# Optimization experiments

Hardware: AMD Instinct MI355X
Metric: run time of the kernel (lower is better)

## Reference

```python
import jax, jax.numpy as jnp
import numpy as np
import math

B, S, E, H = 2, 2048, 768, 12
D = E // H            # head_dim = 64
FFN = 3072            # GeGLU hidden
WIN = 64              # local window size
GLOBAL_IDS = np.array([0])
EPS = 1e-5


def _rope(x):
    # x: [B,H,S,D]; interleaved rotary embedding, theta=10000 (lucidrains RotaryEmbedding)
    d = x.shape[-1]
    s = x.shape[-2]
    inv_freq = 1.0 / (10000.0 ** (jnp.arange(0, d, 2, dtype=jnp.float32) / d))
    freqs = jnp.arange(s, dtype=jnp.float32)[:, None] * inv_freq[None, :]  # [S, D/2]
    freqs = jnp.repeat(freqs, 2, axis=-1)                                   # [S, D]
    cos, sin = jnp.cos(freqs), jnp.sin(freqs)
    xp = x.reshape(x.shape[:-1] + (d // 2, 2))
    x_rot = jnp.stack([-xp[..., 1], xp[..., 0]], axis=-1).reshape(x.shape)
    return x * cos + x_rot * sin


def _layernorm(x, scale, bias):
    mu = jnp.mean(x, axis=-1, keepdims=True)
    var = jnp.mean(jnp.square(x - mu), axis=-1, keepdims=True)
    return (x - mu) * jax.lax.rsqrt(var + EPS) * scale + bias


def setup_inputs() -> dict:
    key = jax.random.key(0)
    ks = jax.random.split(key, 10)
    def xav(k, shape, gain):
        fan_out, fan_in = shape
        std = gain * math.sqrt(2.0 / (fan_in + fan_out))
        return jax.random.normal(k, shape, jnp.float32) * std
    g2 = math.sqrt(2.0)
    g13 = math.sqrt(1.0 / 3.0)
    return {
        "x": jax.random.normal(ks[0], (B, S, E), jnp.float32),
        "rel_pos_bias": jax.random.normal(ks[1], (B, S, S), jnp.float32),
        "mask": jnp.ones((B, S), dtype=bool),
        "wq_w": xav(ks[2], (E, E), g2), "wq_b": jnp.zeros((E,), jnp.float32),
        "wk_w": xav(ks[3], (E, E), g2), "wk_b": jnp.zeros((E,), jnp.float32),
        "wv_w": xav(ks[4], (E, E), g2), "wv_b": jnp.zeros((E,), jnp.float32),
        "fc_w": xav(ks[5], (E, E), g2), "fc_b": jnp.zeros((E,), jnp.float32),
        "pos_coeff": jnp.full((H, 1, 1), 0.01, jnp.float32),
        "gate_w": xav(ks[6], (FFN, E), g13), "gate_b": jnp.zeros((FFN,), jnp.float32),
        "value_w": xav(ks[7], (FFN, E), g2), "value_b": jnp.zeros((FFN,), jnp.float32),
        "down_w": xav(ks[8], (E, FFN), g2), "down_b": jnp.zeros((E,), jnp.float32),
        "ln1_s": jnp.ones((E,), jnp.float32), "ln1_b": jnp.zeros((E,), jnp.float32),
        "ln2_s": jnp.ones((E,), jnp.float32), "ln2_b": jnp.zeros((E,), jnp.float32),
    }


def _sparse_allow(mask):
    # static local-window + global-token pattern, [S,S] bool
    idx = jnp.arange(S)
    allow = jnp.abs(idx[:, None] - idx[None, :]) <= WIN
    gidx = jnp.asarray(GLOBAL_IDS)
    allow = allow.at[gidx, :].set(True)
    allow = allow.at[:, gidx].set(True)
    # combine with padding mask [B,S] broadcast over query rows
    return allow[None, None, :, :] & mask[:, None, None, :]  # [B,1,S,S]


def reference(x, rel_pos_bias, mask, wq_w, wq_b, wk_w, wk_b, wv_w, wv_b,
              fc_w, fc_b, pos_coeff, gate_w, gate_b, value_w, value_b,
              down_w, down_b, ln1_s, ln1_b, ln2_s, ln2_b):
    def heads(t):  # [B,S,E] -> [B,H,S,D]
        return t.reshape(B, S, H, D).transpose(0, 2, 1, 3)

    Q = _rope(heads(x @ wq_w.T + wq_b))
    K = _rope(heads(x @ wk_w.T + wk_b))
    V = heads(x @ wv_w.T + wv_b)

    scores = jnp.einsum('bhqd,bhkd->bhqk', Q, K) / math.sqrt(D)
    scores = scores + pos_coeff[None] * rel_pos_bias[:, None]     # [B,H,S,S]
    allow = _sparse_allow(mask)
    scores = jnp.where(allow, scores, -1e30)
    scores = scores - jnp.max(scores, axis=-1, keepdims=True)
    attn = jax.nn.softmax(scores, axis=-1)
    ctx = jnp.einsum('bhqk,bhkd->bhqd', attn, V)
    ctx = ctx.transpose(0, 2, 1, 3).reshape(B, S, E)
    attn_out = ctx @ fc_w.T + fc_b

    h = _layernorm(x + attn_out, ln1_s, ln1_b)
    gate = jax.nn.gelu(h @ gate_w.T + gate_b, approximate=False)
    ffn = (gate * (h @ value_w.T + value_b)) @ down_w.T + down_b
    return _layernorm(h + ffn, ln2_s, ln2_b)
```

## Files before the change

### kernel.cpp

```cpp
#include <hip/hip_runtime.h>
#include <math.h>

#define B_   2
#define S_   2048
#define E_   768
#define H_   12
#define D_   64
#define FFN_ 3072
#define WIN_ 64
#define MTOT (B_*S_)

typedef unsigned short ushort_t;
typedef unsigned short ushort8 __attribute__((ext_vector_type(8)));
typedef __bf16 bf16x8 __attribute__((ext_vector_type(8)));
typedef float f32x4 __attribute__((ext_vector_type(4)));

__device__ __forceinline__ float b2f(ushort_t u) {
    union { unsigned int i; float f; } c; c.i = ((unsigned int)u) << 16; return c.f;
}
__device__ __forceinline__ ushort_t f2b(float f) {
    union { float f; unsigned int i; } c; c.f = f;
    unsigned int u = c.i;
    return (ushort_t)((u + 0x7fffu + ((u >> 16) & 1u)) >> 16);
}
__device__ __forceinline__ float gelu_f(float g) {
    return 0.5f * g * (1.f + erff(g * 0.70710678118654752440f));
}

typedef const __attribute__((address_space(1))) void* gptr_t;
typedef __attribute__((address_space(3))) void* lptr_t;
__device__ __forceinline__ void gload16(const void* g, void* l) {
    __builtin_amdgcn_global_load_lds((gptr_t)g,
        (lptr_t)(unsigned int)(unsigned long long)l, 16, 0, 0);
}

__global__ __launch_bounds__(256)
void cvt_f32_bf16(const float* __restrict__ in, ushort_t* __restrict__ out, int n8)
{
    const int idx = blockIdx.x * 256 + threadIdx.x;
    if (idx >= n8) return;
    const float4* p = (const float4*)(in + (size_t)idx * 8);
    const float4 a = p[0], b = p[1];
    ushort8 o;
    o[0]=f2b(a.x); o[1]=f2b(a.y); o[2]=f2b(a.z); o[3]=f2b(a.w);
    o[4]=f2b(b.x); o[5]=f2b(b.y); o[6]=f2b(b.z); o[7]=f2b(b.w);
    *(ushort8*)(out + (size_t)idx*8) = o;
}

__global__ __launch_bounds__(256)
void cvt_interleave(const float* __restrict__ gw, const float* __restrict__ vw,
                    ushort_t* __restrict__ out)
{
    const int idx = blockIdx.x*256 + threadIdx.x;
    const int R   = idx / 96, c8 = idx - R*96;
    const int blk = R >> 6, w = R & 63;
    const float* src = (w < 32 ? gw : vw) + (size_t)(blk*32 + (w & 31))*768 + c8*8;
    const float4 a = ((const float4*)src)[0], b = ((const float4*)src)[1];
    ushort8 o;
    o[0]=f2b(a.x); o[1]=f2b(a.y); o[2]=f2b(a.z); o[3]=f2b(a.w);
    o[4]=f2b(b.x); o[5]=f2b(b.y); o[6]=f2b(b.z); o[7]=f2b(b.w);
    *(ushort8*)(out + (size_t)idx*8) = o;
}

__global__ __launch_bounds__(256)
void rope_table(float2* __restrict__ ctab)
{
    const int idx = blockIdx.x*256 + threadIdx.x;
    if (idx >= S_*32) return;
    const int s = idx >> 5, i = idx & 31;
    const float inv = exp2f(-(float)i * (13.287712379549449f/32.0f));
    const float fr = (float)s * inv;
    ctab[idx] = make_float2(cosf(fr), sinf(fr));
}

__global__ __launch_bounds__(256)
void rope_apply(ushort_t* __restrict__ Qb, ushort_t* __restrict__ Kb,
                const float2* __restrict__ ctab)
{
    const int NP4 = MTOT*E_/8;
    int idx = blockIdx.x*256 + threadIdx.x;
    ushort_t* ptr = Qb;
    if (idx >= NP4) { ptr = Kb; idx -= NP4; if (idx >= NP4) return; }
    const size_t p0 = (size_t)idx * 4;
    const int e2 = (int)(p0 % (E_/2));
    const int s  = (int)((p0 / (E_/2)) % S_);
    const int i0 = e2 & 31;
    ushort8 v = *(ushort8*)(ptr + p0*2);
    ushort8 o;
#pragma unroll
    for (int t = 0; t < 4; ++t) {
        const float2 cs = ctab[s*32 + i0 + t];
        const float x0 = b2f(v[2*t]), x1 = b2f(v[2*t+1]);
        o[2*t]   = f2b(x0*cs.x - x1*cs.y);
        o[2*t+1] = f2b(x1*cs.x + x0*cs.y);
    }
    *(ushort8*)(ptr + p0*2) = o;
}

template<int EPI, int BN>
__global__ __launch_bounds__(256)
void gemm_mfma(const ushort_t* __restrict__ A,
               const ushort_t* W0, const float* b0, void* C0,
               const ushort_t* W1, const float* b1, void* C1,
               const ushort_t* W2, const float* b2, void* C2,
               const void* __restrict__ aux, int M, int N, int K)
{
    constexpr int NWC = BN/64, NWR = 4/NWC, WROWS = 128/NWR, MF = WROWS/16;
    const ushort_t* W = W0; const float* bias = b0; void* C = C0;
    if (blockIdx.z == 1) { W = W1; bias = b1; C = C1; }
    else if (blockIdx.z == 2) { W = W2; bias = b2; C = C2; }

    __shared__ __align__(16) ushort_t As[128*32];
    __shared__ __align__(16) ushort_t Bs[BN*32];

    const int tid = threadIdx.x, wv = tid>>6, lane = tid&63;
    const int m0 = blockIdx.y*128, n0 = blockIdx.x*BN;
    const int wr = wv / NWC, wc = wv % NWC;
    const int lr16 = lane & 15, lkb = (lane>>4)<<3;

    f32x4 acc[MF][4];
#pragma unroll
    for (int i=0;i<MF;++i)
#pragma unroll
        for (int j=0;j<4;++j) acc[i][j] = f32x4{0.f,0.f,0.f,0.f};

    const char* Ab = (const char*)(A + (size_t)m0*K);
    const char* Wb = (const char*)(W + (size_t)n0*K);
    const size_t rb = (size_t)K*2;
    const int wbase = wv*1024, lby = lane*16;

    for (int kt = 0; kt < K; kt += 32) {
        const size_t kb = (size_t)kt*2;
        int n_ = wbase + lby;
        gload16(Ab + (size_t)(n_>>6)*rb + kb + (n_&63), (char*)As + wbase);
        n_ += 4096;
        gload16(Ab + (size_t)(n_>>6)*rb + kb + (n_&63), (char*)As + wbase + 4096);
        n_ = wbase + lby;
        gload16(Wb + (size_t)(n_>>6)*rb + kb + (n_&63), (char*)Bs + wbase);
        if (BN == 128) {
            n_ += 4096;
            gload16(Wb + (size_t)(n_>>6)*rb + kb + (n_&63), (char*)Bs + wbase + 4096);
        }
        __syncthreads();
        bf16x8 af[MF], bfr[4];
#pragma unroll
        for (int mf=0; mf<MF; ++mf)
            af[mf] = *(const bf16x8*)&As[(wr*WROWS + mf*16 + lr16)*32 + lkb];
#pragma unroll
        for (int nf=0; nf<4; ++nf)
            bfr[nf] = *(const bf16x8*)&Bs[(wc*64 + nf*16 + lr16)*32 + lkb];
#pragma unroll
        for (int mf=0; mf<MF; ++mf)
#pragma unroll
            for (int nf=0; nf<4; ++nf)
                acc[mf][nf] = __builtin_amdgcn_mfma_f32_16x16x32_bf16(af[mf], bfr[nf], acc[mf][nf], 0,0,0);
        __syncthreads();
    }

    const int colb = n0 + wc*64 + lr16;
    const int rowb = m0 + wr*WROWS + ((lane>>4)<<2);
#pragma unroll
    for (int nf=0; nf<4; ++nf) {
        const int col = colb + nf*16;
        const float bsv = bias[col];
#pragma unroll
        for (int mf=0; mf<MF; ++mf) {
            const int row = rowb + mf*16;
            const f32x4 a = acc[mf][nf];
#pragma unroll
            for (int r=0; r<4; ++r) {
                const size_t off = (size_t)(row+r)*N + col;
                const float v = a[r] + bsv;
                if constexpr (EPI == 0) {
                    ((ushort_t*)C)[off] = f2b(v);
                } else if constexpr (EPI == 1) {
                    ((float*)C)[off] = v + ((const float*)aux)[off];
                } else {
                    if (blockIdx.z == 2) {
                        const int rr = row + r;
                        const size_t toff =
                            (((size_t)(rr >> 11)*H_ + (col >> 6))*64 + (col & 63))*(size_t)S_ + (rr & (S_-1));
                        ((ushort_t*)C)[toff] = f2b(v);
                    } else {
                        ((ushort_t*)C)[off] = f2b(v);
                    }
                }
            }
        }
    }
}

__global__ __launch_bounds__(256, 2)
void gemm_geglu(const ushort_t* __restrict__ A,
                const ushort_t* __restrict__ Wgv,
                const float* __restrict__ bgp,
                const float* __restrict__ bvp,
                ushort_t* __restrict__ C)
{
    constexpr int NT   = 12;
    constexpr int ABY  = 128*128;
    constexpr int BUFB = 2*ABY;
    __shared__ __align__(16) char lds[2*BUFB];

    const int id  = blockIdx.x;
    const int stI = (id & 7)*3 + ((id >> 3) >> 6);
    const int w64 = (id >> 3) & 63;
    const int gy  = (stI/6)*8 + (w64 >> 3);
    const int gx  = (stI%6)*8 + (w64 & 7);
    const int m0 = gy*128, n0 = gx*128;

    const int tid = threadIdx.x, wv = tid>>6, l = tid&63;
    const int wr = wv>>1, wc = wv&1;
    const int lr16 = l & 15, g16b = (l>>4)<<4;
    const int xr = (lr16 & 7) << 4;

    const int lrow = l >> 3;
    const int swzc = ((l & 7) ^ lrow) << 4;
    const char* Agp = (const char*)A   + (size_t)(m0 + wv*32 + lrow)*1536 + swzc;
    const char* Bgp = (const char*)Wgv + (size_t)(n0 + wv*32 + lrow)*1536 + swzc;

    const int rA0 = (wr*64 +  0 + lr16)*128, rA1 = (wr*64 + 16 + lr16)*128;
    const int rA2 = (wr*64 + 32 + lr16)*128, rA3 = (wr*64 + 48 + lr16)*128;
    const int rB0 = ABY + (wc*64 +  0 + lr16)*128, rB1 = ABY + (wc*64 + 16 + lr16)*128;
    const int rB2 = ABY + (wc*64 + 32 + lr16)*128, rB3 = ABY + (wc*64 + 48 + lr16)*128;
    const int ck0 = g16b ^ xr, ck1 = (64 + g16b) ^ xr;

    f32x4 acc[4][4];
#pragma unroll
    for (int i=0;i<4;++i)
#pragma unroll
        for (int j=0;j<4;++j) acc[i][j] = f32x4{0.f,0.f,0.f,0.f};

#define STG(tt, cb) { \
    char* dA = lds + (cb)*BUFB + wv*4096; \
    char* dB = lds + (cb)*BUFB + ABY + wv*4096; \
    const size_t ko = (size_t)(tt)*128; \
    gload16(Agp + ko,           dA); \
    gload16(Agp + ko +  8*1536, dA + 1024); \
    gload16(Agp + ko + 16*1536, dA + 2048); \
    gload16(Agp + ko + 24*1536, dA + 3072); \
    gload16(Bgp + ko,           dB); \
    gload16(Bgp + ko +  8*1536, dB + 1024); \
    gload16(Bgp + ko + 16*1536, dB + 2048); \
    gload16(Bgp + ko + 24*1536, dB + 3072); }

    STG(0, 0);
    __syncthreads();

    int c = 0;
#pragma unroll 1
    for (int t = 0; t < NT; ++t) {
        if (t < NT-1) STG(t+1, c^1);
        const char* Lb = lds + c*BUFB;
        const bf16x8 a0 = *(const bf16x8*)(Lb + rA0 + ck0);
        const bf16x8 a1 = *(const bf16x8*)(Lb + rA1 + ck0);
        const bf16x8 a2 = *(const bf16x8*)(Lb + rA2 + ck0);
        const bf16x8 a3 = *(const bf16x8*)(Lb + rA3 + ck0);
        const bf16x8 b0 = *(const bf16x8*)(Lb + rB0 + ck0);
        const bf16x8 b1 = *(const bf16x8*)(Lb + rB1 + ck0);
        const bf16x8 b2 = *(const bf16x8*)(Lb + rB2 + ck0);
        const bf16x8 b3 = *(const bf16x8*)(Lb + rB3 + ck0);
        const bf16x8 e0 = *(const bf16x8*)(Lb + rA0 + ck1);
        const bf16x8 e1 = *(const bf16x8*)(Lb + rA1 + ck1);
        const bf16x8 e2 = *(const bf16x8*)(Lb + rA2 + ck1);
        const bf16x8 e3 = *(const bf16x8*)(Lb + rA3 + ck1);
        const bf16x8 f0 = *(const bf16x8*)(Lb + rB0 + ck1);
        const bf16x8 f1 = *(const bf16x8*)(Lb + rB1 + ck1);
        const bf16x8 f2 = *(const bf16x8*)(Lb + rB2 + ck1);
        const bf16x8 f3 = *(const bf16x8*)(Lb + rB3 + ck1);
        __builtin_amdgcn_s_setprio(1);
        acc[0][0] = __builtin_amdgcn_mfma_f32_16x16x32_bf16(a0, b0, acc[0][0], 0,0,0);
        acc[1][0] = __builtin_amdgcn_mfma_f32_16x16x32_bf16(a1, b0, acc[1][0], 0,0,0);
        acc[2][0] = __builtin_amdgcn_mfma_f32_16x16x32_bf16(a2, b0, acc[2][0], 0,0,0);
        acc[3][0] = __builtin_amdgcn_mfma_f32_16x16x32_bf16(a3, b0, acc[3][0], 0,0,0);
        acc[0][1] = __builtin_amdgcn_mfma_f32_16x16x32_bf16(a0, b1, acc[0][1], 0,0,0);
        acc[1][1] = __builtin_amdgcn_mfma_f32_16x16x32_bf16(a1, b1, acc[1][1], 0,0,0);
        acc[2][1] = __builtin_amdgcn_mfma_f32_16x16x32_bf16(a2, b1, acc[2][1], 0,0,0);
        acc[3][1] = __builtin_amdgcn_mfma_f32_16x16x32_bf16(a3, b1, acc[3][1], 0,0,0);
        acc[0][2] = __builtin_amdgcn_mfma_f32_16x16x32_bf16(a0, b2, acc[0][2], 0,0,0);
        acc[1][2] = __builtin_amdgcn_mfma_f32_16x16x32_bf16(a1, b2, acc[1][2], 0,0,0);
        acc[2][2] = __builtin_amdgcn_mfma_f32_16x16x32_bf16(a2, b2, acc[2][2], 0,0,0);
        acc[3][2] = __builtin_amdgcn_mfma_f32_16x16x32_bf16(a3, b2, acc[3][2], 0,0,0);
        acc[0][3] = __builtin_amdgcn_mfma_f32_16x16x32_bf16(a0, b3, acc[0][3], 0,0,0);
        acc[1][3] = __builtin_amdgcn_mfma_f32_16x16x32_bf16(a1, b3, acc[1][3], 0,0,0);
        acc[2][3] = __builtin_amdgcn_mfma_f32_16x16x32_bf16(a2, b3, acc[2][3], 0,0,0);
        acc[3][3] = __builtin_amdgcn_mfma_f32_16x16x32_bf16(a3, b3, acc[3][3], 0,0,0);
        acc[0][0] = __builtin_amdgcn_mfma_f32_16x16x32_bf16(e0, f0, acc[0][0], 0,0,0);
        acc[1][0] = __builtin_amdgcn_mfma_f32_16x16x32_bf16(e1, f0, acc[1][0], 0,0,0);
        acc[2][0] = __builtin_amdgcn_mfma_f32_16x16x32_bf16(e2, f0, acc[2][0], 0,0,0);
        acc[3][0] = __builtin_amdgcn_mfma_f32_16x16x32_bf16(e3, f0, acc[3][0], 0,0,0);
        acc[0][1] = __builtin_amdgcn_mfma_f32_16x16x32_bf16(e0, f1, acc[0][1], 0,0,0);
        acc[1][1] = __builtin_amdgcn_mfma_f32_16x16x32_bf16(e1, f1, acc[1][1], 0,0,0);
        acc[2][1] = __builtin_amdgcn_mfma_f32_16x16x32_bf16(e2, f1, acc[2][1], 0,0,0);
        acc[3][1] = __builtin_amdgcn_mfma_f32_16x16x32_bf16(e3, f1, acc[3][1], 0,0,0);
        acc[0][2] = __builtin_amdgcn_mfma_f32_16x16x32_bf16(e0, f2, acc[0][2], 0,0,0);
        acc[1][2] = __builtin_amdgcn_mfma_f32_16x16x32_bf16(e1, f2, acc[1][2], 0,0,0);
        acc[2][2] = __builtin_amdgcn_mfma_f32_16x16x32_bf16(e2, f2, acc[2][2], 0,0,0);
        acc[3][2] = __builtin_amdgcn_mfma_f32_16x16x32_bf16(e3, f2, acc[3][2], 0,0,0);
        acc[0][3] = __builtin_amdgcn_mfma_f32_16x16x32_bf16(e0, f3, acc[0][3], 0,0,0);
        acc[1][3] = __builtin_amdgcn_mfma_f32_16x16x32_bf16(e1, f3, acc[1][3], 0,0,0);
        acc[2][3] = __builtin_amdgcn_mfma_f32_16x16x32_bf16(e2, f3, acc[2][3], 0,0,0);
        acc[3][3] = __builtin_amdgcn_mfma_f32_16x16x32_bf16(e3, f3, acc[3][3], 0,0,0);
        __builtin_amdgcn_s_setprio(0);
        __syncthreads();
        c ^= 1;
    }
#undef STG

    const int colb = gx*64 + wc*32 + lr16;
    const int rowb = m0 + wr*64 + ((l>>4)<<2);
#pragma unroll
    for (int nf=0; nf<2; ++nf) {
        const int col = colb + nf*16;
        const float bgv = bgp[col], bvv = bvp[col];
#pragma unroll
        for (int mf=0; mf<4; ++mf) {
            const int row = rowb + mf*16;
            const f32x4 gq = acc[mf][nf];
            const f32x4 vq = acc[mf][nf+2];
#pragma unroll
            for (int r=0; r<4; ++r) {
                C[(size_t)(row+r)*3072 + col] =
                    f2b(gelu_f(gq[r] + bgv) * (vq[r] + bvv));
            }
        }
    }
}

__global__ __launch_bounds__(256)
void attn_mfma(const ushort_t* __restrict__ Qb, const ushort_t* __restrict__ Kb,
               const ushort_t* __restrict__ Vt, const float* __restrict__ rel,
               const float* __restrict__ pos_coeff, ushort_t* __restrict__ ctx)
{
    __shared__ __align__(16) ushort_t P_lds[4][16][160];
    const int id = blockIdx.x;
    const int h  = id % H_;
    const int qb = (id / H_) & 31;
    const int b  = id / (H_*32);
    const int wv = threadIdx.x >> 6, l = threadIdx.x & 63;
    const int qw = qb*64 + wv*16;
    const int g  = l >> 4, ql = l & 15;
    const int q  = qw + ql;

    int klo = qw - 64;
    if (klo < 0) klo = 0;
    if (klo > S_-160) klo = S_-160;
    const bool addg = (klo > 0);
    const float pc = pos_coeff[h];

    const ushort_t* qbp = Qb + ((size_t)(b*S_ + qw))*E_ + h*D_ + (size_t)ql*E_ + g*8;
    const bf16x8 qf0 = *(const bf16x8*)(qbp);
    const bf16x8 qf1 = *(const bf16x8*)(qbp + 32);

    float sg = -1e30f, pg = 0.f;
    const float* relrow = rel + ((size_t)(b*S_ + q))*S_;
    if (addg) {
        const ushort_t* k0p = Kb + (size_t)(b*S_)*E_ + h*D_ + g*8;
        const bf16x8 k00 = *(const bf16x8*)(k0p);
        const bf16x8 k01 = *(const bf16x8*)(k0p + 32);
        float part = 0.f;
#pragma unroll
        for (int t = 0; t < 8; ++t) {
            part = fmaf((float)k00[t], (float)qf0[t], part);
            part = fmaf((float)k01[t], (float)qf1[t], part);
        }
        part += __shfl_xor(part, 16);
        part += __shfl_xor(part, 32);
        sg = part*0.125f + pc*relrow[0];
    }

    f32x4 sc_[10];
#pragma unroll
    for (int f = 0; f < 10; ++f) sc_[f] = f32x4{0.f,0.f,0.f,0.f};
    const ushort_t* kbp = Kb + ((size_t)(b*S_ + klo))*E_ + h*D_;
#pragma unroll
    for (int f = 0; f < 10; ++f) {
        const ushort_t* kr = kbp + (size_t)(16*f + ql)*E_ + g*8;
        const bf16x8 kf0 = *(const bf16x8*)(kr);
        const bf16x8 kf1 = *(const bf16x8*)(kr + 32);
        sc_[f] = __builtin_amdgcn_mfma_f32_16x16x32_bf16(kf0, qf0, sc_[f], 0,0,0);
        sc_[f] = __builtin_amdgcn_mfma_f32_16x16x32_bf16(kf1, qf1, sc_[f], 0,0,0);
    }

#pragma unroll
    for (int f = 0; f < 10; ++f) {
#pragma unroll
        for (int r = 0; r < 4; ++r) {
            const int slot = 16*f + 4*g + r;
            const int key  = klo + slot;
            const int dd   = key - q;
            const bool ok  = (dd <= WIN_ && dd >= -WIN_) || (key == 0);
            const float v  = sc_[f][r]*0.125f + pc*relrow[key];
            sc_[f][r] = ok ? v : -1e30f;
        }
    }

    float mx = sg;
#pragma unroll
    for (int f = 0; f < 10; ++f)
#pragma unroll
        for (int r = 0; r < 4; ++r) mx = fmaxf(mx, sc_[f][r]);
    mx = fmaxf(mx, __shfl_xor(mx, 16));
    mx = fmaxf(mx, __shfl_xor(mx, 32));

    float ls = 0.f;
#pragma unroll
    for (int f = 0; f < 10; ++f)
#pragma unroll
        for (int r = 0; r < 4; ++r) {
            const float p = __expf(sc_[f][r] - mx);
            sc_[f][r] = p; ls += p;
        }
    if (addg) pg = __expf(sg - mx);
    ls += (g == 0) ? pg : 0.f;
    ls += __shfl_xor(ls, 16);
    ls += __shfl_xor(ls, 32);
    const float inv = 1.f / ls;

#pragma unroll
    for (int f = 0; f < 10; ++f)
#pragma unroll
        for (int r = 0; r < 4; ++r)
            P_lds[wv][ql][16*f + 4*g + r] = f2b(sc_[f][r]);
    __syncthreads();

    f32x4 acc_c[4];
#pragma unroll
    for (int df = 0; df < 4; ++df) acc_c[df] = f32x4{0.f,0.f,0.f,0.f};
    const ushort_t* vtb = Vt + ((size_t)(b*H_ + h)*64)*(size_t)S_;
#pragma unroll
    for (int s5 = 0; s5 < 5; ++s5) {
        const bf16x8 pf = *(const bf16x8*)&P_lds[wv][ql][32*s5 + 8*g];
#pragma unroll
        for (int df = 0; df < 4; ++df) {
            const bf16x8 vtf = *(const bf16x8*)(vtb + (size_t)(df*16 + ql)*S_ + klo + 32*s5 + g*8);
            acc_c[df] = __builtin_amdgcn_mfma_f32_16x16x32_bf16(vtf, pf, acc_c[df], 0,0,0);
        }
    }

    if (addg) {
#pragma unroll
        for (int df = 0; df < 4; ++df)
#pragma unroll
            for (int r = 0; r < 4; ++r)
                acc_c[df][r] = fmaf(pg, b2f(vtb[(size_t)(df*16 + g*4 + r)*S_]), acc_c[df][r]);
    }

    if (q != 0) {
        ushort_t* cb = ctx + ((size_t)(b*S_ + q))*E_ + h*D_;
#pragma unroll
        for (int df = 0; df < 4; ++df)
#pragma unroll
            for (int r = 0; r < 4; ++r)
                cb[df*16 + g*4 + r] = f2b(acc_c[df][r] * inv);
    }
}

__global__ __launch_bounds__(256)
void attn_global(const ushort_t* __restrict__ Qb, const ushort_t* __restrict__ Kb,
                 const ushort_t* __restrict__ Vt, const float* __restrict__ rel,
                 const float* __restrict__ pos_coeff, ushort_t* __restrict__ ctx)
{
    __shared__ float sc[S_];
    __shared__ float sq[D_];
    __shared__ float red[4];
    __shared__ float pacc[4][D_];
    const int tid = threadIdx.x, wv = tid>>6, lane = tid&63;
    const int id = blockIdx.x, h = id % H_, b = id / H_;

    if (tid < 64) sq[tid] = b2f(Qb[(size_t)(b*S_)*E_ + h*D_ + tid]);
    __syncthreads();

    const float pc = pos_coeff[h];
    const ushort_t* kbase = Kb + (size_t)b*S_*E_ + h*D_;
    const float* relrow = rel + (size_t)b*S_*S_;
    const int g = lane >> 2, sl = lane & 3;

    for (int jb = wv*16; jb < S_; jb += 64) {
        const int j = jb + g;
        const ushort_t* kr = kbase + (size_t)j*E_ + sl*16;
        const ushort8 k0 = *(const ushort8*)kr;
        const ushort8 k1 = *(const ushort8*)(kr + 8);
        const float* qv = &sq[sl*16];
        float partial = 0.f;
#pragma unroll
        for (int t = 0; t < 8; ++t) partial = fmaf(b2f(k0[t]), qv[t], partial);
#pragma unroll
        for (int t = 0; t < 8; ++t) partial = fmaf(b2f(k1[t]), qv[t+8], partial);
        partial += __shfl_xor(partial, 1);
        partial += __shfl_xor(partial, 2);
        if (sl == 0) sc[j] = partial*0.125f + pc*relrow[j];
    }
    __syncthreads();

    float mx = -1e30f;
#pragma unroll
    for (int i = 0; i < 8; ++i) mx = fmaxf(mx, sc[tid + 256*i]);
#pragma unroll
    for (int off = 32; off > 0; off >>= 1) mx = fmaxf(mx, __shfl_xor(mx, off));
    if (lane == 0) red[wv] = mx;
    __syncthreads();
    mx = fmaxf(fmaxf(red[0], red[1]), fmaxf(red[2], red[3]));

    float sum = 0.f;
#pragma unroll
    for (int i = 0; i < 8; ++i) {
        const float p = __expf(sc[tid + 256*i] - mx);
        sc[tid + 256*i] = p; sum += p;
    }
#pragma unroll
    for (int off = 32; off > 0; off >>= 1) sum += __shfl_xor(sum, off);
    __syncthreads();
    if (lane == 0) red[wv] = sum;
    __syncthreads();
    const float inv = 1.f / (red[0]+red[1]+red[2]+red[3]);

    const ushort_t* vtrow = Vt + ((size_t)(b*H_ + h)*64 + lane)*(size_t)S_;
    float acc = 0.f;
    for (int j0 = wv*512; j0 < wv*512 + 512; j0 += 8) {
        const ushort8 v8 = *(const ushort8*)&vtrow[j0];
#pragma unroll
        for (int t = 0; t < 8; ++t) acc = fmaf(sc[j0+t], b2f(v8[t]), acc);
    }
    pacc[wv][lane] = acc;
    __syncthreads();
    if (tid < 64) {
        const float r = (pacc[0][tid]+pacc[1][tid]+pacc[2][tid]+pacc[3][tid]) * inv;
        ctx[(size_t)(b*S_)*E_ + h*D_ + tid] = f2b(r);
    }
}

template<bool WB>
__global__ __launch_bounds__(256)
void ln_kernel(const float* __restrict__ in, const float* __restrict__ gam,
               const float* __restrict__ bet, float* __restrict__ out,
               ushort_t* __restrict__ outb)
{
    const int row = blockIdx.x;
    const float* r = in + (size_t)row * E_;
    const int tid = threadIdx.x;
    const float v0 = r[tid], v1 = r[tid+256], v2 = r[tid+512];
    float s  = v0+v1+v2;
    float ss = v0*v0+v1*v1+v2*v2;
#pragma unroll
    for (int off = 32; off > 0; off >>= 1) {
        s  += __shfl_xor(s, off);
        ss += __shfl_xor(ss, off);
    }
    __shared__ float rs[4], rss[4];
    const int wv = tid >> 6, lane = tid & 63;
    if (lane == 0) { rs[wv] = s; rss[wv] = ss; }
    __syncthreads();
    s  = rs[0]+rs[1]+rs[2]+rs[3];
    ss = rss[0]+rss[1]+rss[2]+rss[3];
    const float mu  = s * (1.f/E_);
    const float var = ss * (1.f/E_) - mu*mu;
    const float rstd = rsqrtf(var + 1e-5f);
    float* o = out + (size_t)row * E_;
    const float o0 = (v0-mu)*rstd*gam[tid    ] + bet[tid    ];
    const float o1 = (v1-mu)*rstd*gam[tid+256] + bet[tid+256];
    const float o2 = (v2-mu)*rstd*gam[tid+512] + bet[tid+512];
    o[tid] = o0; o[tid+256] = o1; o[tid+512] = o2;
    if constexpr (WB) {
        ushort_t* ob = outb + (size_t)row * E_;
        ob[tid] = f2b(o0); ob[tid+256] = f2b(o1); ob[tid+512] = f2b(o2);
    }
}

extern "C" void kernel_launch(void* const* d_in, const int* in_sizes, int n_in,
                              void* d_out, int out_size, void* d_ws, size_t ws_size,
                              hipStream_t stream)
{
    const float* x      = (const float*)d_in[0];
    const float* rel    = (const float*)d_in[1];
    const float* wq_w   = (const float*)d_in[3];
    const float* wq_b   = (const float*)d_in[4];
    const float* wk_w   = (const float*)d_in[5];
    const float* wk_b   = (const float*)d_in[6];
    const float* wv_w   = (const float*)d_in[7];
    const float* wv_b   = (const float*)d_in[8];
    const float* fc_w   = (const float*)d_in[9];
    const float* fc_b   = (const float*)d_in[10];
    const float* pos_c  = (const float*)d_in[11];
    const float* gate_w = (const float*)d_in[12];
    const float* gate_b = (const float*)d_in[13];
    const float* value_w= (const float*)d_in[14];
    const float* value_b= (const float*)d_in[15];
    const float* down_w = (const float*)d_in[16];
    const float* down_b = (const float*)d_in[17];
    const float* ln1_s  = (const float*)d_in[18];
    const float* ln1_b  = (const float*)d_in[19];
    const float* ln2_s  = (const float*)d_in[20];
    const float* ln2_b  = (const float*)d_in[21];
    float* out = (float*)d_out;

    char* W = (char*)d_ws;
    ushort_t* Qb     = (ushort_t*)(W + 0);
    ushort_t* Kb     = (ushort_t*)(W + 6291456);
    ushort_t* Vt     = (ushort_t*)(W + 12582912);
    ushort_t* Cxb    = (ushort_t*)(W + 18874368);
    ushort_t* GpB    = (ushort_t*)(W + 0);
    ushort_t* Xb     = (ushort_t*)(W + 25165824);
    ushort_t* wqb    = (ushort_t*)(W + 31457280);
    ushort_t* wkb    = (ushort_t*)(W + 32636928);
    ushort_t* wvb    = (ushort_t*)(W + 33816576);
    ushort_t* fcb    = (ushort_t*)(W + 34996224);
    ushort_t* Wgv    = (ushort_t*)(W + 25165824);
    ushort_t* downb  = (ushort_t*)(W + 34996224);
    float*    AO     = (float*)   (W + 39714816);
    float*    Hb     = (float*)   (W + 52297728);
    ushort_t* Hbb    = (ushort_t*)(W + 64880640);
    float2*   ctab   = (float2*)  (W + 71172096);

    cvt_f32_bf16<<<1536, 256, 0, stream>>>(x, Xb, MTOT*E_/8);
    cvt_f32_bf16<<<288,  256, 0, stream>>>(wq_w, wqb, E_*E_/8);
    cvt_f32_bf16<<<288,  256, 0, stream>>>(wk_w, wkb, E_*E_/8);
    cvt_f32_bf16<<<288,  256, 0, stream>>>(wv_w, wvb, E_*E_/8);
    cvt_f32_bf16<<<288,  256, 0, stream>>>(fc_w, fcb, E_*E_/8);
    rope_table<<<(S_*32+255)/256, 256, 0, stream>>>(ctab);

    gemm_mfma<2,128><<<dim3(E_/128, MTOT/128, 3), 256, 0, stream>>>(
        Xb, wqb, wq_b, Qb, wkb, wk_b, Kb, wvb, wv_b, Vt, nullptr, MTOT, E_, E_);

    cvt_interleave<<<2304, 256, 0, stream>>>(gate_w, value_w, Wgv);

    rope_apply<<<3072, 256, 0, stream>>>(Qb, Kb, ctab);

    attn_mfma<<<B_*H_*(S_/64), 256, 0, stream>>>(Qb, Kb, Vt, rel, pos_c, Cxb);
    attn_global<<<B_*H_, 256, 0, stream>>>(Qb, Kb, Vt, rel, pos_c, Cxb);

    gemm_mfma<1,64><<<dim3(E_/64, MTOT/128, 1), 256, 0, stream>>>(
        Cxb, fcb, fc_b, AO, nullptr, nullptr, nullptr, nullptr, nullptr, nullptr,
        x, MTOT, E_, E_);

    cvt_f32_bf16<<<1152, 256, 0, stream>>>(down_w, downb, E_*FFN_/8);

    ln_kernel<true><<<MTOT, 256, 0, stream>>>(AO, ln1_s, ln1_b, Hb, Hbb);

    gemm_geglu<<<dim3(1536), 256, 0, stream>>>(Hbb, Wgv, gate_b, value_b, GpB);

    gemm_mfma<1,64><<<dim3(E_/64, MTOT/128, 1), 256, 0, stream>>>(
        GpB, downb, down_b, AO, nullptr, nullptr, nullptr, nullptr, nullptr, nullptr,
        Hb, MTOT, E_, FFN_);

    ln_kernel<false><<<MTOT, 256, 0, stream>>>(AO, ln2_s, ln2_b, out, nullptr);
}
```

Measured before the change: 266.7 us.

## Split-K the down projection into two halves and reduce inside final layernorm

Replaces the down-projection GEMM (K=3072, only 384 blocks of 128x64) with a split-K=2 kernel launched as 768 blocks, giving more parallelism across CUs. The first K-half writes fp32 plus bias, the second writes fp16 partials into the freed Hbb buffer. A new layernorm kernel sums both partials with the residual before normalizing. The block index is remapped across groups of eight, and the fp16 partial adds rounding error plus an extra memory round trip.

```diff
diff --git a/kernel.cpp b/kernel.cpp
--- a/kernel.cpp
+++ b/kernel.cpp
@@ -14,6 +14,7 @@
 typedef unsigned short ushort8 __attribute__((ext_vector_type(8)));
 typedef __bf16 bf16x8 __attribute__((ext_vector_type(8)));
 typedef float f32x4 __attribute__((ext_vector_type(4)));
+typedef _Float16 half_t;
 
 __device__ __forceinline__ float b2f(ushort_t u) {
     union { unsigned int i; float f; } c; c.i = ((unsigned int)u) << 16; return c.f;
@@ -327,6 +328,123 @@
     }
 }
 
+__global__ __launch_bounds__(256, 3)
+void gemm_down(const ushort_t* __restrict__ A,
+               const ushort_t* __restrict__ Wd,
+               const float* __restrict__ bias,
+               float* __restrict__ P0,
+               half_t* __restrict__ P1)
+{
+    constexpr int NT   = 24;
+    constexpr int ABY  = 128*128;
+    constexpr int BBY  = 64*128;
+    constexpr int BUFB = ABY + BBY;
+    __shared__ __align__(16) char lds[2*BUFB];
+
+    const int id   = blockIdx.x;
+    const int work = (id & 7)*96 + (id >> 3);
+    const int z    = work / 384;
+    const int r    = work - z*384;
+    const int gy   = r / 12, gx = r - gy*12;
+    const int m0 = gy*128, n0 = gx*64;
+
+    const int tid = threadIdx.x, wv = tid>>6, l = tid&63;
+    const int wr = wv>>1, wc = wv&1;
+    const int lr16 = l & 15, g16b = (l>>4)<<4;
+    const int xr = (lr16 & 7) << 4;
+
+    const int lrow = l >> 3;
+    const int swzc = ((l & 7) ^ lrow) << 4;
+    const size_t kbase = (size_t)z*3072;
+    const char* Agp = (const char*)A  + (size_t)(m0 + wv*32 + lrow)*6144 + kbase + swzc;
+    const char* Bgp = (const char*)Wd + (size_t)(n0 + wv*16 + lrow)*6144 + kbase + swzc;
+
+    const int rA0 = (wr*64 +  0 + lr16)*128, rA1 = (wr*64 + 16 + lr16)*128;
+    const int rA2 = (wr*64 + 32 + lr16)*128, rA3 = (wr*64 + 48 + lr16)*128;
+    const int rB0 = ABY + (wc*32 +  0 + lr16)*128;
+    const int rB1 = ABY + (wc*32 + 16 + lr16)*128;
+    const int ck0 = g16b ^ xr, ck1 = (64 + g16b) ^ xr;
+
+    f32x4 acc[4][2];
+#pragma unroll
+    for (int i=0;i<4;++i)
+#pragma unroll
+        for (int j=0;j<2;++j) acc[i][j] = f32x4{0.f,0.f,0.f,0.f};
+
+#define STGD(tt, cb) { \
+    char* dA = lds + (cb)*BUFB + wv*4096; \
+    char* dB = lds + (cb)*BUFB + ABY + wv*2048; \
+    const size_t ko = (size_t)(tt)*128; \
+    gload16(Agp + ko,           dA); \
+    gload16(Agp + ko +  8*6144, dA + 1024); \
+    gload16(Agp + ko + 16*6144, dA + 2048); \
+    gload16(Agp + ko + 24*6144, dA + 3072); \
+    gload16(Bgp + ko,           dB); \
+    gload16(Bgp + ko +  8*6144, dB + 1024); }
+
+    STGD(0, 0);
+    __syncthreads();
+
+    int c = 0;
+#pragma unroll 1
+    for (int t = 0; t < NT; ++t) {
+        if (t < NT-1) STGD(t+1, c^1);
+        const char* Lb = lds + c*BUFB;
+        const bf16x8 a0 = *(const bf16x8*)(Lb + rA0 + ck0);
+        const bf16x8 a1 = *(const bf16x8*)(Lb + rA1 + ck0);
+        const bf16x8 a2 = *(const bf16x8*)(Lb + rA2 + ck0);
+        const bf16x8 a3 = *(const bf16x8*)(Lb + rA3 + ck0);
+        const bf16x8 b0 = *(const bf16x8*)(Lb + rB0 + ck0);
+        const bf16x8 b1 = *(const bf16x8*)(Lb + rB1 + ck0);
+        const bf16x8 e0 = *(const bf16x8*)(Lb + rA0 + ck1);
+        const bf16x8 e1 = *(const bf16x8*)(Lb + rA1 + ck1);
+        const bf16x8 e2 = *(const bf16x8*)(Lb + rA2 + ck1);
+        const bf16x8 e3 = *(const bf16x8*)(Lb + rA3 + ck1);
+        const bf16x8 f0 = *(const bf16x8*)(Lb + rB0 + ck1);
+        const bf16x8 f1 = *(const bf16x8*)(Lb + rB1 + ck1);
+        __builtin_amdgcn_s_setprio(1);
+        acc[0][0] = __builtin_amdgcn_mfma_f32_16x16x32_bf16(a0, b0, acc[0][0], 0,0,0);
+        acc[1][0] = __builtin_amdgcn_mfma_f32_16x16x32_bf16(a1, b0, acc[1][0], 0,0,0);
+        acc[2][0] = __builtin_amdgcn_mfma_f32_16x16x32_bf16(a2, b0, acc[2][0], 0,0,0);
+        acc[3][0] = __builtin_amdgcn_mfma_f32_16x16x32_bf16(a3, b0, acc[3][0], 0,0,0);
+        acc[0][1] = __builtin_amdgcn_mfma_f32_16x16x32_bf16(a0, b1, acc[0][1], 0,0,0);
+        acc[1][1] = __builtin_amdgcn_mfma_f32_16x16x32_bf16(a1, b1, acc[1][1], 0,0,0);
+        acc[2][1] = __builtin_amdgcn_mfma_f32_16x16x32_bf16(a2, b1, acc[2][1], 0,0,0);
+        acc[3][1] = __builtin_amdgcn_mfma_f32_16x16x32_bf16(a3, b1, acc[3][1], 0,0,0);
+        acc[0][0] = __builtin_amdgcn_mfma_f32_16x16x32_bf16(e0, f0, acc[0][0], 0,0,0);
+        acc[1][0] = __builtin_amdgcn_mfma_f32_16x16x32_bf16(e1, f0, acc[1][0], 0,0,0);
+        acc[2][0] = __builtin_amdgcn_mfma_f32_16x16x32_bf16(e2, f0, acc[2][0], 0,0,0);
+        acc[3][0] = __builtin_amdgcn_mfma_f32_16x16x32_bf16(e3, f0, acc[3][0], 0,0,0);
+        acc[0][1] = __builtin_amdgcn_mfma_f32_16x16x32_bf16(e0, f1, acc[0][1], 0,0,0);
+        acc[1][1] = __builtin_amdgcn_mfma_f32_16x16x32_bf16(e1, f1, acc[1][1], 0,0,0);
+        acc[2][1] = __builtin_amdgcn_mfma_f32_16x16x32_bf16(e2, f1, acc[2][1], 0,0,0);
+        acc[3][1] = __builtin_amdgcn_mfma_f32_16x16x32_bf16(e3, f1, acc[3][1], 0,0,0);
+        __builtin_amdgcn_s_setprio(0);
+        __syncthreads();
+        c ^= 1;
+    }
+#undef STGD
+
+    const int colb = n0 + wc*32 + lr16;
+    const int rowb = m0 + wr*64 + ((l>>4)<<2);
+#pragma unroll
+    for (int nf=0; nf<2; ++nf) {
+        const int col = colb + nf*16;
+        const float bsv = bias[col];
+#pragma unroll
+        for (int mf=0; mf<4; ++mf) {
+            const int row = rowb + mf*16;
+            const f32x4 a = acc[mf][nf];
+#pragma unroll
+            for (int rr=0; rr<4; ++rr) {
+                const size_t off = (size_t)(row+rr)*E_ + col;
+                if (z == 0) P0[off] = a[rr] + bsv;
+                else        P1[off] = (half_t)a[rr];
+            }
+        }
+    }
+}
+
 __global__ __launch_bounds__(256)
 void attn_mfma(const ushort_t* __restrict__ Qb, const ushort_t* __restrict__ Kb,
                const ushort_t* __restrict__ Vt, const float* __restrict__ rel,
@@ -565,6 +683,39 @@
         ushort_t* ob = outb + (size_t)row * E_;
         ob[tid] = f2b(o0); ob[tid+256] = f2b(o1); ob[tid+512] = f2b(o2);
     }
+}
+
+__global__ __launch_bounds__(256)
+void ln3_kernel(const float* __restrict__ p0, const half_t* __restrict__ p1,
+                const float* __restrict__ res, const float* __restrict__ gam,
+                const float* __restrict__ bet, float* __restrict__ out)
+{
+    const int row = blockIdx.x;
+    const size_t base = (size_t)row * E_;
+    const int tid = threadIdx.x;
+    const float v0 = p0[base+tid]     + (float)p1[base+tid]     + res[base+tid];
+    const float v1 = p0[base+tid+256] + (float)p1[base+tid+256] + res[base+tid+256];
+    const float v2 = p0[base+tid+512] + (float)p1[base+tid+512] + res[base+tid+512];
+    float s  = v0+v1+v2;
+    float ss = v0*v0+v1*v1+v2*v2;
+#pragma unroll
+    for (int off = 32; off > 0; off >>= 1) {
+        s  += __shfl_xor(s, off);
+        ss += __shfl_xor(ss, off);
+    }
+    __shared__ float rs[4], rss[4];
+    const int wv = tid >> 6, lane = tid & 63;
+    if (lane == 0) { rs[wv] = s; rss[wv] = ss; }
+    __syncthreads();
+    s  = rs[0]+rs[1]+rs[2]+rs[3];
+    ss = rss[0]+rss[1]+rss[2]+rss[3];
+    const float mu  = s * (1.f/E_);
+    const float var = ss * (1.f/E_) - mu*mu;
+    const float rstd = rsqrtf(var + 1e-5f);
+    float* o = out + base;
+    o[tid]     = (v0-mu)*rstd*gam[tid    ] + bet[tid    ];
+    o[tid+256] = (v1-mu)*rstd*gam[tid+256] + bet[tid+256];
+    o[tid+512] = (v2-mu)*rstd*gam[tid+512] + bet[tid+512];
 }
 
 extern "C" void kernel_launch(void* const* d_in, const int* in_sizes, int n_in,
@@ -610,6 +761,7 @@
     float*    AO     = (float*)   (W + 39714816);
     float*    Hb     = (float*)   (W + 52297728);
     ushort_t* Hbb    = (ushort_t*)(W + 64880640);
+    half_t*   P1h    = (half_t*)  (W + 64880640);
     float2*   ctab   = (float2*)  (W + 71172096);
 
     cvt_f32_bf16<<<1536, 256, 0, stream>>>(x, Xb, MTOT*E_/8);
@@ -639,9 +791,7 @@
 
     gemm_geglu<<<dim3(1536), 256, 0, stream>>>(Hbb, Wgv, gate_b, value_b, GpB);
 
-    gemm_mfma<1,64><<<dim3(E_/64, MTOT/128, 1), 256, 0, stream>>>(
-        GpB, downb, down_b, AO, nullptr, nullptr, nullptr, nullptr, nullptr, nullptr,
-        Hb, MTOT, E_, FFN_);
-
-    ln_kernel<false><<<MTOT, 256, 0, stream>>>(AO, ln2_s, ln2_b, out, nullptr);
-}
+    gemm_down<<<dim3(768), 256, 0, stream>>>(GpB, downb, down_b, AO, P1h);
+
+    ln3_kernel<<<MTOT, 256, 0, stream>>>(AO, P1h, Hb, ln2_s, ln2_b, out);
+}
```

After: 236.2 us. 11.4% less time.
